# Kernel tuning notes

Hardware: AMD Instinct MI355X
Metric: run time of the kernel (lower is better)

The kernel has to match this reference:

```python
import jax, jax.numpy as jnp
import numpy as np

T, D_MODEL = 2048, 6144
NH, NKV, HD = 48, 8, 128
THETA, CAP = 10000.0, 30.0


def setup_inputs() -> dict:
    key = jax.random.key(0)
    k1, k2, k3 = jax.random.split(key, 3)
    return {
        "positions": jnp.arange(T, dtype=jnp.int32),
        "hidden_states": jax.random.normal(k1, (T, D_MODEL), jnp.float32),
        "w_qkv": jax.random.normal(k2, (D_MODEL, (NH + 2 * NKV) * HD), jnp.float32) * 0.02,
        "w_o": jax.random.normal(k3, (NH * HD, D_MODEL), jnp.float32) * 0.02,
    }


def _rope_neox(positions, x):
    # x: [T, h, HD]; neox-style: rotate concatenated halves
    half = HD // 2
    inv_freq = 1.0 / (THETA ** (jnp.arange(0, HD, 2, dtype=jnp.float32) / HD))  # [half]
    freqs = positions.astype(jnp.float32)[:, None] * inv_freq  # [T, half]
    cos = jnp.cos(freqs)[:, None, :]  # [T,1,half]
    sin = jnp.sin(freqs)[:, None, :]
    x1, x2 = x[..., :half], x[..., half:]
    return jnp.concatenate([x1 * cos - x2 * sin, x2 * cos + x1 * sin], axis=-1)


def reference(positions, hidden_states, w_qkv, w_o):
    qkv = hidden_states @ w_qkv  # [T, (NH+2*NKV)*HD]
    q, k, v = jnp.split(qkv, [NH * HD, NH * HD + NKV * HD], axis=-1)
    q = q.reshape(T, NH, HD)
    k = k.reshape(T, NKV, HD)
    v = v.reshape(T, NKV, HD)
    q = _rope_neox(positions, q)
    k = _rope_neox(positions, k)
    # GQA: expand kv heads to query heads
    g = NH // NKV
    k = jnp.repeat(k, g, axis=1)  # [T, NH, HD]
    v = jnp.repeat(v, g, axis=1)
    scale = HD ** -0.5
    logits = jnp.einsum('thd,shd->hts', q, k) * scale  # [NH, T, T]
    logits = CAP * jnp.tanh(logits / CAP)  # tanh logit softcapping
    causal = positions[:, None] >= positions[None, :]  # [T, T]
    logits = jnp.where(causal[None, :, :], logits, -jnp.inf)
    probs = jax.nn.softmax(logits, axis=-1)
    out = jnp.einsum('hts,shd->thd', probs, v)  # [T, NH, HD]
    out = out.reshape(T, NH * HD)
    return out @ w_o
```

## Files before the change

kernel.cpp:

```cpp
#include <hip/hip_runtime.h>
#include <hip/hip_bf16.h>
#include <stdint.h>

#define TSEQ   2048
#define DMODEL 6144
#define NHEADS 48
#define NKVH   8
#define HDIM   128
#define QKVC   8192
#define GRP    6

typedef __attribute__((ext_vector_type(8))) short short8;
typedef __attribute__((ext_vector_type(4))) float f32x4;


__device__ __forceinline__ unsigned short f2b(float f) {
  union { float f; unsigned int u; } v; v.f = f;
  unsigned int u = v.u;
  unsigned int r = (u + 0x7FFFu + ((u >> 16) & 1u)) >> 16;
  return (unsigned short)r;
}

__device__ __forceinline__ float b2f(unsigned short s) {
  union { unsigned int u; float f; } v; v.u = ((unsigned int)s) << 16;
  return v.f;
}

#if __has_builtin(__builtin_amdgcn_exp2f)
#define EXP2(x) __builtin_amdgcn_exp2f(x)
#else
#define EXP2(x) exp2f(x)
#endif
#if __has_builtin(__builtin_amdgcn_rcpf)
#define RCP(x) __builtin_amdgcn_rcpf(x)
#else
#define RCP(x) (1.0f / (x))
#endif

typedef const __attribute__((address_space(1))) void* as1_cvp;
typedef __attribute__((address_space(3))) void* as3_vp;

__device__ __forceinline__ void gload_lds16(const void* g, void* l) {
  __builtin_amdgcn_global_load_lds(
      (as1_cvp)(uintptr_t)g,
      (as3_vp)(unsigned int)(uintptr_t)l, 16, 0, 0);
}

#define LGKMC(n) do { asm volatile("s_waitcnt lgkmcnt(" #n ")" ::: "memory"); \
                      __builtin_amdgcn_sched_barrier(0); } while (0)
#define VMC(n) do { asm volatile("s_waitcnt vmcnt(" #n ")" ::: "memory"); \
                    __builtin_amdgcn_sched_barrier(0); } while (0)
#define BARR  do { asm volatile("s_barrier" ::: "memory"); } while (0)


__global__ __launch_bounds__(256) void k_cvt(const float* __restrict__ in,
                                             unsigned short* __restrict__ outp, int n) {
  int i = (blockIdx.x * 256 + threadIdx.x) * 8;
  if (i + 7 < n) {
    float4 va = *(const float4*)(in + i);
    float4 vb = *(const float4*)(in + i + 4);
    union { unsigned short s[8]; uint4 u; } o;
    o.s[0] = f2b(va.x); o.s[1] = f2b(va.y); o.s[2] = f2b(va.z); o.s[3] = f2b(va.w);
    o.s[4] = f2b(vb.x); o.s[5] = f2b(vb.y); o.s[6] = f2b(vb.z); o.s[7] = f2b(vb.w);
    *(uint4*)(outp + i) = o.u;
  }
}

__global__ __launch_bounds__(256) void k_tr2(const float* __restrict__ in, long istr, long zin,
                                             unsigned short* __restrict__ out, long ostr, long zout) {
  __shared__ unsigned short tile[64][68];
  const int tid = threadIdx.x;
  const int br = blockIdx.y * 64;
  const int bc = blockIdx.x * 64;
  in  += (size_t)blockIdx.z * zin;
  out += (size_t)blockIdx.z * zout;
  const int row = tid >> 4;
  const int c4  = (tid & 15) * 4;
#pragma unroll
  for (int p = 0; p < 4; ++p) {
    const int r = p * 16 + row;
    float4 v = *(const float4*)(in + (size_t)(br + r) * istr + bc + c4);
    tile[r][c4 + 0] = f2b(v.x);
    tile[r][c4 + 1] = f2b(v.y);
    tile[r][c4 + 2] = f2b(v.z);
    tile[r][c4 + 3] = f2b(v.w);
  }
  __syncthreads();
#pragma unroll
  for (int p = 0; p < 4; ++p) {
    const int r = p * 16 + row;
    union { unsigned short s[4]; uint2 u; } o;
    o.s[0] = tile[c4 + 0][r];
    o.s[1] = tile[c4 + 1][r];
    o.s[2] = tile[c4 + 2][r];
    o.s[3] = tile[c4 + 3][r];
    *(uint2*)(out + (size_t)(bc + r) * ostr + br + c4) = o.u;
  }
}

__global__ __launch_bounds__(256) void k_tr2b(const unsigned short* __restrict__ in, long istr, long zin,
                                              unsigned short* __restrict__ out, long ostr, long zout) {
  __shared__ unsigned short tile[64][68];
  const int tid = threadIdx.x;
  const int br = blockIdx.y * 64;
  const int bc = blockIdx.x * 64;
  in  += (size_t)blockIdx.z * zin;
  out += (size_t)blockIdx.z * zout;
  const int row = tid >> 4;
  const int c4  = (tid & 15) * 4;
#pragma unroll
  for (int p = 0; p < 4; ++p) {
    const int r = p * 16 + row;
    union { unsigned short s[4]; uint2 u; } v;
    v.u = *(const uint2*)(in + (size_t)(br + r) * istr + bc + c4);
    tile[r][c4 + 0] = v.s[0];
    tile[r][c4 + 1] = v.s[1];
    tile[r][c4 + 2] = v.s[2];
    tile[r][c4 + 3] = v.s[3];
  }
  __syncthreads();
#pragma unroll
  for (int p = 0; p < 4; ++p) {
    const int r = p * 16 + row;
    union { unsigned short s[4]; uint2 u; } o;
    o.s[0] = tile[c4 + 0][r];
    o.s[1] = tile[c4 + 1][r];
    o.s[2] = tile[c4 + 2][r];
    o.s[3] = tile[c4 + 3][r];
    *(uint2*)(out + (size_t)(bc + r) * ostr + br + c4) = o.u;
  }
}

__global__ void k_trig(const int* __restrict__ pos, float* __restrict__ cs,
                       float* __restrict__ sn) {
  int t = blockIdx.x, i = threadIdx.x;
  float p = (float)pos[t];
  float inv = EXP2(-(float)(2 * i) * (1.0f / 128.0f) * 13.287712379549449f);
  float f = p * inv;
  cs[t * 64 + i] = cosf(f);
  sn[t * 64 + i] = sinf(f);
}


#define READ_A(mh, aa) do { \
  _Pragma("unroll") for (int m = 0; m < 4; ++m) \
  _Pragma("unroll") for (int ks = 0; ks < 2; ++ks) \
    aa[m][ks] = *(const short8*)(LA + (wm * 128 + (mh) * 64 + m * 16 + lr) * 128 \
                                 + ((ks * 64 + lkb) ^ lsw)); } while (0)

#define READ_B(nh, bb) do { \
  _Pragma("unroll") for (int n2 = 0; n2 < 2; ++n2) \
  _Pragma("unroll") for (int ks = 0; ks < 2; ++ks) \
    bb[n2][ks] = *(const short8*)(LB + (wn * 64 + (nh) * 32 + n2 * 16 + lr) * 128 \
                                  + ((ks * 64 + lkb) ^ lsw)); } while (0)

#define CLUSTER(mh, nh, aa, bb) do { \
  __builtin_amdgcn_s_setprio(1); \
  _Pragma("unroll") for (int m = 0; m < 4; ++m) \
  _Pragma("unroll") for (int n2 = 0; n2 < 2; ++n2) \
  _Pragma("unroll") for (int ks = 0; ks < 2; ++ks) \
    acc[(mh) * 4 + m][(nh) * 2 + n2] = __builtin_amdgcn_mfma_f32_16x16x32_bf16( \
        aa[m][ks], bb[n2][ks], acc[(mh) * 4 + m][(nh) * 2 + n2], 0, 0, 0); \
  __builtin_amdgcn_s_setprio(0); } while (0)

#define STAGE_A(kt, bb) do { \
  _Pragma("unroll") for (int i = 0; i < 4; ++i) \
    gload_lds16(Asrc + (size_t)(kt) * 64 + (size_t)i * 64 * K, \
                lds + (bb) * 65536 + F + i * 8192); } while (0)

#define STAGE_B(kt, bb) do { \
  _Pragma("unroll") for (int i = 0; i < 4; ++i) \
    gload_lds16(Bsrc + (size_t)(kt) * 64 + (size_t)i * 64 * K, \
                lds + (bb) * 65536 + 32768 + F + i * 8192); } while (0)

template <typename OutT>
__global__ __launch_bounds__(512, 2) void k_gemm8(const unsigned short* __restrict__ A,
                                                  const unsigned short* __restrict__ Bt,
                                                  OutT* __restrict__ C,
                                                  int M, int N, int K) {
  extern __shared__ __align__(16) unsigned char lds[];
  const int tid  = threadIdx.x;
  const int lane = tid & 63;
  const int wave = tid >> 6;
  const int wm = wave >> 2;
  const int wn = wave & 3;
  const int lr  = lane & 15;
  const int lkb = (lane >> 4) * 16;
  const int li4 = (lane >> 4) * 4;
  const int lsw = (lane & 7) << 4;

  const int mt = M >> 8;
  const int nt = N >> 8;
  const int Cx = nt >> 3;
  const int lin = blockIdx.x;
  const int xcd = lin & 7;
  const int r   = lin >> 3;
  const int m0  = (r % mt) << 8;
  const int n0  = (xcd * Cx + r / mt) << 8;

  const int F   = tid * 16;
  const int r0  = F >> 7;
  const int cbs = (F & 127) ^ ((r0 & 7) << 4);
  const unsigned short* Asrc = A  + (size_t)(m0 + r0) * K + (cbs >> 1);
  const unsigned short* Bsrc = Bt + (size_t)(n0 + r0) * K + (cbs >> 1);

  const int NT = K >> 6;

  f32x4 acc[8][4];
#pragma unroll
  for (int i = 0; i < 8; ++i)
#pragma unroll
    for (int j = 0; j < 4; ++j) acc[i][j] = (f32x4){0.f, 0.f, 0.f, 0.f};

  STAGE_A(0, 0);
  STAGE_B(0, 0);
  STAGE_A(1, 1);
  VMC(4);
  BARR;

  for (int t = 0; t < NT; ++t) {
    const int cur = t & 1;
    const unsigned char* LA = lds + cur * 65536;
    const unsigned char* LB = LA + 32768;
    short8 a0[4][2], a1[4][2], b0[2][2], b1[2][2];

    READ_A(0, a0);
    READ_B(0, b0);
    if (t + 1 < NT) STAGE_B(t + 1, cur ^ 1);
    READ_B(1, b1);
    READ_A(1, a1);

    LGKMC(12);
    CLUSTER(0, 0, a0, b0);
    LGKMC(8);
    CLUSTER(0, 1, a0, b1);
    LGKMC(0);
    CLUSTER(1, 0, a1, b0);
    BARR;
    if (t + 2 < NT) STAGE_A(t + 2, cur);
    CLUSTER(1, 1, a1, b1);
    if (t + 2 < NT) { VMC(4); } else { VMC(0); }
    BARR;
  }

#pragma unroll
  for (int mh = 0; mh < 2; ++mh)
#pragma unroll
    for (int m = 0; m < 4; ++m)
#pragma unroll
      for (int nh = 0; nh < 2; ++nh)
#pragma unroll
        for (int n2 = 0; n2 < 2; ++n2)
#pragma unroll
          for (int i = 0; i < 4; ++i) {
            int row = m0 + wm * 128 + mh * 64 + m * 16 + li4 + i;
            int col = n0 + wn * 64 + nh * 32 + n2 * 16 + lr;
            float v = acc[mh * 4 + m][nh * 2 + n2][i];
            if constexpr (sizeof(OutT) == 2)
              C[(size_t)row * N + col] = (OutT)f2b(v);
            else
              C[(size_t)row * N + col] = (OutT)v;
          }
}


__global__ __launch_bounds__(256) void k_rope(const unsigned short* __restrict__ qkv,
                                              const float* __restrict__ cs,
                                              const float* __restrict__ sn,
                                              unsigned short* __restrict__ Q,
                                              unsigned short* __restrict__ K) {
  const int t = blockIdx.x;
  const int tid = threadIdx.x;
  const unsigned short* row = qkv + (size_t)t * QKVC;
  const float* c = cs + t * 64;
  const float* s = sn + t * 64;
  for (int p = tid; p < 56 * 16; p += 256) {
    const int h = p >> 4, q4 = (p & 15) * 4;
    const unsigned short* src = row + h * 128;
    union { unsigned short sh[4]; uint2 u; } x1u, x2u;
    x1u.u = *(const uint2*)(src + q4);
    x2u.u = *(const uint2*)(src + 64 + q4);
    float4 cc = *(const float4*)(c + q4);
    float4 ss = *(const float4*)(s + q4);
    unsigned short* dst = (h < NHEADS)
        ? Q + ((size_t)h * TSEQ + t) * HDIM
        : K + ((size_t)(h - NHEADS) * TSEQ + t) * HDIM;
    float x10 = b2f(x1u.sh[0]), x11 = b2f(x1u.sh[1]),
          x12 = b2f(x1u.sh[2]), x13 = b2f(x1u.sh[3]);
    float x20 = b2f(x2u.sh[0]), x21 = b2f(x2u.sh[1]),
          x22 = b2f(x2u.sh[2]), x23 = b2f(x2u.sh[3]);
    union { unsigned short sh[4]; uint2 u; } o1, o2;
    o1.sh[0] = f2b(x10 * cc.x - x20 * ss.x);
    o1.sh[1] = f2b(x11 * cc.y - x21 * ss.y);
    o1.sh[2] = f2b(x12 * cc.z - x22 * ss.z);
    o1.sh[3] = f2b(x13 * cc.w - x23 * ss.w);
    o2.sh[0] = f2b(x20 * cc.x + x10 * ss.x);
    o2.sh[1] = f2b(x21 * cc.y + x11 * ss.y);
    o2.sh[2] = f2b(x22 * cc.z + x12 * ss.z);
    o2.sh[3] = f2b(x23 * cc.w + x13 * ss.w);
    *(uint2*)(dst + q4) = o1.u;
    *(uint2*)(dst + 64 + q4) = o2.u;
  }
}


__global__ __launch_bounds__(256, 3) void k_attn2(const unsigned short* __restrict__ Q,
                                                  const unsigned short* __restrict__ K,
                                                  const unsigned short* __restrict__ V,
                                                  unsigned short* __restrict__ O) {
  __shared__ __align__(16) unsigned char KsB[16384];
  __shared__ __align__(16) unsigned char VsB[16384];
  __shared__ __align__(16) unsigned char PsB[4][2048];

  const int lin = blockIdx.x;
  const int g   = lin & 7;
  const int rr  = lin >> 3;
  const int hg  = rr % 6;
  const int pr  = rr / 6;
  const int h   = g * 6 + hg;
  const int tid = threadIdx.x, wave = tid >> 6, lane = tid & 63;
  const int lr = lane & 15, lk = (lane >> 4) * 8, li4 = (lane >> 4) * 4;
  const unsigned short* Qh = Q + (size_t)h * (TSEQ * HDIM);
  const unsigned char*  Kb = (const unsigned char*)(K + (size_t)g * (TSEQ * HDIM));
  const unsigned char*  Vb = (const unsigned char*)(V + (size_t)g * (TSEQ * HDIM));
  unsigned char* Pw = PsB[wave];

  for (int half = 0; half < 2; ++half) {
    const int j  = half ? (31 - pr) : pr;
    const int t0 = j * 64 + wave * 16;
    const int nst = j + 1;

    short8 qf[4];
#pragma unroll
    for (int ks = 0; ks < 4; ++ks)
      qf[ks] = *(const short8*)(Qh + (size_t)(t0 + lr) * HDIM + ks * 32 + lk);

    f32x4 oacc[8];
#pragma unroll
    for (int n = 0; n < 8; ++n) oacc[n] = (f32x4){0.f, 0.f, 0.f, 0.f};
    float rs4[4] = {0.f, 0.f, 0.f, 0.f};

    for (int st = 0; st < nst; ++st) {
      const int s0 = st * 64;
#pragma unroll
      for (int c = 0; c < 4; ++c) {
        const int FF = tid * 16 + c * 4096;
        const int krow = FF >> 8;
        const int kcol = (FF & 255) ^ ((krow & 7) << 4);
        gload_lds16(Kb + (size_t)(s0 + krow) * 256 + kcol, KsB + FF);
        const int vrow = FF >> 7;
        const int vcol = (FF & 127) ^ ((vrow & 7) << 4);
        gload_lds16(Vb + (size_t)vrow * (TSEQ * 2) + (size_t)s0 * 2 + vcol, VsB + FF);
      }
      __syncthreads();

      f32x4 sacc[4];
#pragma unroll
      for (int n = 0; n < 4; ++n) sacc[n] = (f32x4){0.f, 0.f, 0.f, 0.f};
#pragma unroll
      for (int ks = 0; ks < 4; ++ks) {
        short8 kf[4];
#pragma unroll
        for (int n = 0; n < 4; ++n) {
          const int row = n * 16 + lr;
          kf[n] = *(const short8*)(KsB + row * 256 + ((ks * 64 + lk * 2) ^ ((row & 7) << 4)));
        }
#pragma unroll
        for (int n = 0; n < 4; ++n)
          sacc[n] = __builtin_amdgcn_mfma_f32_16x16x32_bf16(qf[ks], kf[n], sacc[n], 0, 0, 0);
      }

      const bool lastst = (st == nst - 1);
#pragma unroll
      for (int n = 0; n < 4; ++n)
#pragma unroll
        for (int i = 0; i < 4; ++i) {
          float sv = sacc[n][i] * 0.08838834764831845f;
          float e = EXP2(sv * 0.09617966939259757f);
          float p = EXP2(-86.5617024533378f * RCP(e + 1.0f));
          if (lastst && (s0 + n * 16 + lr > t0 + li4 + i)) p = 0.f;
          rs4[i] += p;
          const int prow = li4 + i;
          *(unsigned short*)(Pw + prow * 128 +
              (((n * 16 + lr) * 2) ^ ((prow & 7) << 4))) = f2b(p);
        }

#pragma unroll
      for (int ks2 = 0; ks2 < 2; ++ks2) {
        short8 pf = *(const short8*)(Pw + lr * 128 +
                         (((ks2 * 32 + lk) * 2) ^ ((lr & 7) << 4)));
        short8 vf[8];
#pragma unroll
        for (int n = 0; n < 8; ++n) {
          const int row = n * 16 + lr;
          vf[n] = *(const short8*)(VsB + row * 128 + ((ks2 * 64 + lk * 2) ^ ((row & 7) << 4)));
        }
#pragma unroll
        for (int n = 0; n < 8; ++n)
          oacc[n] = __builtin_amdgcn_mfma_f32_16x16x32_bf16(pf, vf[n], oacc[n], 0, 0, 0);
      }
      __syncthreads();
    }

    float inv4[4];
#pragma unroll
    for (int i = 0; i < 4; ++i) {
      float v = rs4[i];
      v += __shfl_xor(v, 1, 64);
      v += __shfl_xor(v, 2, 64);
      v += __shfl_xor(v, 4, 64);
      v += __shfl_xor(v, 8, 64);
      inv4[i] = RCP(v);
    }
#pragma unroll
    for (int n = 0; n < 8; ++n)
#pragma unroll
      for (int i = 0; i < 4; ++i)
        O[(size_t)(t0 + li4 + i) * DMODEL + h * HDIM + n * 16 + lr] =
            f2b(oacc[n][i] * inv4[i]);
  }
}


extern "C" void kernel_launch(void* const* d_in, const int* in_sizes, int n_in,
                              void* d_out, int out_size, void* d_ws, size_t ws_size,
                              hipStream_t stream) {
  const int*   pos  = (const int*)d_in[0];
  const float* hid  = (const float*)d_in[1];
  const float* wqkv = (const float*)d_in[2];
  const float* wo   = (const float*)d_in[3];
  float* out = (float*)d_out;
  char* ws = (char*)d_ws;

  const size_t O_XB   = 0;
  const size_t O_WQT  = 25165824;
  const size_t O_WOT  = 125829120;
  const size_t O_QKV  = 201326592;
  const size_t O_TRIG = 268435456;

  unsigned short* Xb  = (unsigned short*)(ws + O_XB);
  unsigned short* Wqt = (unsigned short*)(ws + O_WQT);
  unsigned short* Wot = (unsigned short*)(ws + O_WOT);
  unsigned short* QKVb = (unsigned short*)(ws + O_QKV);
  float* CS  = (float*)(ws + O_TRIG);
  float* SN  = CS + TSEQ * 64;
  unsigned short* Qr = Wqt;
  unsigned short* Kr = Wqt + (size_t)NHEADS * TSEQ * HDIM;
  unsigned short* Vt = Kr + (size_t)NKVH * TSEQ * HDIM;
  unsigned short* AO = Xb;

  hipFuncSetAttribute((const void*)k_gemm8<unsigned short>,
                      hipFuncAttributeMaxDynamicSharedMemorySize, 131072);
  hipFuncSetAttribute((const void*)k_gemm8<float>,
                      hipFuncAttributeMaxDynamicSharedMemorySize, 131072);

  k_cvt<<<(TSEQ * DMODEL) / (256 * 8), 256, 0, stream>>>(hid, Xb, TSEQ * DMODEL);
  k_tr2<<<dim3(QKVC / 64, DMODEL / 64, 1), 256, 0, stream>>>(wqkv, QKVC, 0, Wqt, DMODEL, 0);
  k_tr2<<<dim3(DMODEL / 64, DMODEL / 64, 1), 256, 0, stream>>>(wo, DMODEL, 0, Wot, DMODEL, 0);
  k_trig<<<TSEQ, 64, 0, stream>>>(pos, CS, SN);

  k_gemm8<unsigned short><<<(TSEQ / 256) * (QKVC / 256), 512, 131072, stream>>>(
      Xb, Wqt, QKVb, TSEQ, QKVC, DMODEL);
  k_rope<<<TSEQ, 256, 0, stream>>>(QKVb, CS, SN, Qr, Kr);
  k_tr2b<<<dim3(HDIM / 64, TSEQ / 64, NKVH), 256, 0, stream>>>(
      QKVb + (size_t)(DMODEL + NKVH * HDIM), QKVC, HDIM,
      Vt, TSEQ, (size_t)HDIM * TSEQ);
  k_attn2<<<768, 256, 0, stream>>>(Qr, Kr, Vt, AO);
  k_gemm8<float><<<(TSEQ / 256) * (DMODEL / 256), 512, 131072, stream>>>(
      AO, Wot, out, TSEQ, DMODEL, DMODEL);
}
```

Before: 539.9 us.

## Double-buffer K/V tiles in attention kernel to overlap loads with compute

```diff
diff --git a/kernel.cpp b/kernel.cpp
--- a/kernel.cpp
+++ b/kernel.cpp
@@ -304,12 +304,12 @@
 }
 
 
-__global__ __launch_bounds__(256, 3) void k_attn2(const unsigned short* __restrict__ Q,
+__global__ __launch_bounds__(256, 2) void k_attn3(const unsigned short* __restrict__ Q,
                                                   const unsigned short* __restrict__ K,
                                                   const unsigned short* __restrict__ V,
                                                   unsigned short* __restrict__ O) {
-  __shared__ __align__(16) unsigned char KsB[16384];
-  __shared__ __align__(16) unsigned char VsB[16384];
+  __shared__ __align__(16) unsigned char KsB[2][16384];
+  __shared__ __align__(16) unsigned char VsB[2][16384];
   __shared__ __align__(16) unsigned char PsB[4][2048];
 
   const int lin = blockIdx.x;
@@ -325,6 +325,18 @@
   const unsigned char*  Vb = (const unsigned char*)(V + (size_t)g * (TSEQ * HDIM));
   unsigned char* Pw = PsB[wave];
 
+#define STAGE_KV(st_, b_) do { \
+  const int s_ = (st_) * 64; \
+  _Pragma("unroll") for (int c = 0; c < 4; ++c) { \
+    const int FF = tid * 16 + c * 4096; \
+    const int krow = FF >> 8; \
+    const int kcol = (FF & 255) ^ ((krow & 7) << 4); \
+    gload_lds16(Kb + (size_t)(s_ + krow) * 256 + kcol, KsB[b_] + FF); \
+    const int vrow = FF >> 7; \
+    const int vcol = (FF & 127) ^ ((vrow & 7) << 4); \
+    gload_lds16(Vb + (size_t)vrow * (TSEQ * 2) + (size_t)s_ * 2 + vcol, VsB[b_] + FF); \
+  } } while (0)
+
   for (int half = 0; half < 2; ++half) {
     const int j  = half ? (31 - pr) : pr;
     const int t0 = j * 64 + wave * 16;
@@ -340,20 +352,17 @@
     for (int n = 0; n < 8; ++n) oacc[n] = (f32x4){0.f, 0.f, 0.f, 0.f};
     float rs4[4] = {0.f, 0.f, 0.f, 0.f};
 
+    STAGE_KV(0, 0);
+    VMC(0);
+    BARR;
+
     for (int st = 0; st < nst; ++st) {
+      const int cur = st & 1;
+      if (st + 1 < nst) STAGE_KV(st + 1, cur ^ 1);
+
+      const unsigned char* Ks = KsB[cur];
+      const unsigned char* Vs = VsB[cur];
       const int s0 = st * 64;
-#pragma unroll
-      for (int c = 0; c < 4; ++c) {
-        const int FF = tid * 16 + c * 4096;
-        const int krow = FF >> 8;
-        const int kcol = (FF & 255) ^ ((krow & 7) << 4);
-        gload_lds16(Kb + (size_t)(s0 + krow) * 256 + kcol, KsB + FF);
-        const int vrow = FF >> 7;
-        const int vcol = (FF & 127) ^ ((vrow & 7) << 4);
-        gload_lds16(Vb + (size_t)vrow * (TSEQ * 2) + (size_t)s0 * 2 + vcol, VsB + FF);
-      }
-      __syncthreads();
-
       f32x4 sacc[4];
 #pragma unroll
       for (int n = 0; n < 4; ++n) sacc[n] = (f32x4){0.f, 0.f, 0.f, 0.f};
@@ -363,7 +372,7 @@
 #pragma unroll
         for (int n = 0; n < 4; ++n) {
           const int row = n * 16 + lr;
-          kf[n] = *(const short8*)(KsB + row * 256 + ((ks * 64 + lk * 2) ^ ((row & 7) << 4)));
+          kf[n] = *(const short8*)(Ks + row * 256 + ((ks * 64 + lk * 2) ^ ((row & 7) << 4)));
         }
 #pragma unroll
         for (int n = 0; n < 4; ++n)
@@ -393,13 +402,15 @@
 #pragma unroll
         for (int n = 0; n < 8; ++n) {
           const int row = n * 16 + lr;
-          vf[n] = *(const short8*)(VsB + row * 128 + ((ks2 * 64 + lk * 2) ^ ((row & 7) << 4)));
+          vf[n] = *(const short8*)(Vs + row * 128 + ((ks2 * 64 + lk * 2) ^ ((row & 7) << 4)));
         }
 #pragma unroll
         for (int n = 0; n < 8; ++n)
           oacc[n] = __builtin_amdgcn_mfma_f32_16x16x32_bf16(pf, vf[n], oacc[n], 0, 0, 0);
       }
-      __syncthreads();
+
+      VMC(0);
+      BARR;
     }
 
     float inv4[4];
@@ -418,7 +429,9 @@
       for (int i = 0; i < 4; ++i)
         O[(size_t)(t0 + li4 + i) * DMODEL + h * HDIM + n * 16 + lr] =
             f2b(oacc[n][i] * inv4[i]);
-  }
+    BARR;
+  }
+#undef STAGE_KV
 }
 
 
@@ -465,7 +478,7 @@
   k_tr2b<<<dim3(HDIM / 64, TSEQ / 64, NKVH), 256, 0, stream>>>(
       QKVb + (size_t)(DMODEL + NKVH * HDIM), QKVC, HDIM,
       Vt, TSEQ, (size_t)HDIM * TSEQ);
-  k_attn2<<<768, 256, 0, stream>>>(Qr, Kr, Vt, AO);
+  k_attn3<<<768, 256, 0, stream>>>(Qr, Kr, Vt, AO);
   k_gemm8<float><<<(TSEQ / 256) * (DMODEL / 256), 512, 131072, stream>>>(
       AO, Wot, out, TSEQ, DMODEL, DMODEL);
 }
```

Measured after the change: 541.9 us. Within noise of the previous version (+0.4%).
